# Performance work log

Measured on AMD Instinct MI355X. Metric: run time of the kernel, lower is better.

The kernel has to match this reference:

```python
import jax, jax.numpy as jnp
import numpy as np

DIM = 128
HEADS = 8
HEAD_DIM = DIM // HEADS
PE_DIM = 48
TEMP = 10000.0
WIN = 2
NUM_VALUES = WIN * WIN
SCALE = HEAD_DIM ** -0.5
TWO_PI = 2.0 * np.pi
EPS = 1e-6


def _interleave_sincos(p):
    # p [..., nf] -> interleaved sin(even)/cos(odd), matching torch stack+flatten
    s = jnp.sin(p[..., 0::2])
    c = jnp.cos(p[..., 1::2])
    return jnp.stack((s, c), axis=-1).reshape(p.shape)


def _dim_t(num_pos_feats):
    i = np.arange(num_pos_feats)
    return jnp.asarray(TEMP ** (2.0 * (i // 2) / num_pos_feats), dtype=jnp.float32)


def window_position_bias():
    nf = PE_DIM // 2
    ye = jnp.arange(WIN, dtype=jnp.float32)  # cumsum(ones)-1 along h
    xe = jnp.arange(WIN, dtype=jnp.float32)
    ye = ye / (ye[-1] + EPS) * TWO_PI
    xe = xe / (xe[-1] + EPS) * TWO_PI
    dt = _dim_t(nf)
    pos_y = ye[:, None, None] / dt
    pos_x = xe[None, :, None] / dt
    pos_y = jnp.broadcast_to(pos_y, (WIN, WIN, nf))
    pos_x = jnp.broadcast_to(pos_x, (WIN, WIN, nf))
    pe = jnp.concatenate((_interleave_sincos(pos_y), _interleave_sincos(pos_x)), axis=-1)
    return pe.reshape(NUM_VALUES, PE_DIM)


def points_position_encoding(points):
    # points [n, hw, 2] fractional offsets -> [n, hw, PE_DIM]
    nf = PE_DIM // 2
    ye = points[..., 0] / (WIN + EPS) * TWO_PI
    xe = points[..., 1] / (WIN + EPS) * TWO_PI
    dt = _dim_t(nf)
    pos_y = _interleave_sincos(ye[..., None] / dt)
    pos_x = _interleave_sincos(xe[..., None] / dt)
    return jnp.concatenate((pos_y, pos_x), axis=-1)


def setup_inputs() -> dict:
    key = jax.random.key(0)
    ks = jax.random.split(key, 12)
    n, c, h, w = 2, 48, 192, 192
    y = jax.random.normal(ks[0], (n, c, h, w), jnp.float32)
    x = jax.random.normal(ks[1], (n, c, h, w), jnp.float32)
    conv_w = jax.random.normal(ks[2], (1, 2 * PE_DIM, 3, 3), jnp.float32) * 0.05
    conv_b = jnp.zeros((1,), jnp.float32)
    q_w = jax.random.normal(ks[3], (PE_DIM, DIM), jnp.float32) * (PE_DIM ** -0.5)
    q_b = jnp.zeros((DIM,), jnp.float32)
    k_w = jax.random.normal(ks[4], (PE_DIM, DIM), jnp.float32) * (PE_DIM ** -0.5)
    k_b = jnp.zeros((DIM,), jnp.float32)
    v_w = jax.random.normal(ks[5], (PE_DIM, DIM), jnp.float32) * (PE_DIM ** -0.5)
    v_b = jnp.zeros((DIM,), jnp.float32)
    return {"y": y, "x": x, "conv_w": conv_w, "conv_b": conv_b,
            "q_w": q_w, "q_b": q_b, "k_w": k_w, "k_b": k_b, "v_w": v_w, "v_b": v_b}


def reference(y, x, conv_w, conv_b, q_w, q_b, k_w, k_b, v_w, v_b):
    n, c, h, w = x.shape
    hw = h * w
    # per-pixel horizontal offset from both feature maps
    off = jax.lax.conv_general_dilated(
        jnp.concatenate([y, x], axis=1), conv_w, (1, 1), ((1, 1), (1, 1)),
        dimension_numbers=("NCHW", "OIHW", "NCHW")) + conv_b[None, :, None, None]
    off = jnp.transpose(off, (0, 2, 3, 1)) * (2.0 / w)  # [n,h,w,1]

    gh, gw = jnp.meshgrid(jnp.arange(h, dtype=x.dtype), jnp.arange(w, dtype=x.dtype), indexing="ij")
    # flow.flip(-1) puts the offset on the w coordinate only
    grid_wrp = jnp.stack(
        (jnp.broadcast_to(gh, (n, h, w)),
         gw[None] + off[..., 0]), axis=-1)                      # [n,h,w,2]
    flr = jnp.floor(grid_wrp)
    frac = (grid_wrp - flr).reshape(n, hw, 2)
    flr = flr.reshape(n, hw, 2)

    widx = jnp.array([[0, 0], [0, 1], [1, 0], [1, 1]], dtype=x.dtype)  # window_idx_offset
    g4 = (flr[:, :, None, :] + widx).reshape(n, hw * NUM_VALUES, 2)

    idx0 = jnp.clip(g4[..., 0], 0, h - 1).astype(jnp.int32)
    idx1 = jnp.clip(g4[..., 1], 0, w - 1).astype(jnp.int32)
    lin = idx1 + w * idx0                                      # [n, hw*4]
    wrp = jnp.take_along_axis(y.reshape(n, c, hw), lin[:, None, :], axis=2)  # [n,c,hw*4]
    wrp = jnp.transpose(wrp, (0, 2, 1))                        # [n, hw*4, c]

    # pe_dim // c == 1 tiling; add window position bias per pixel
    pb = window_position_bias()                                # [4, PE_DIM]
    wrp = (wrp.reshape(n, hw, NUM_VALUES, PE_DIM) + pb).reshape(n, hw * NUM_VALUES, PE_DIM)

    x_flat = jnp.transpose(x.reshape(n, c, hw), (0, 2, 1))     # [n, hw, c]
    x_in = x_flat + points_position_encoding(frac)

    nhw = n * hw
    q = (x_in @ q_w + q_b).reshape(nhw, HEADS, HEAD_DIM)
    k = (wrp @ k_w + k_b).reshape(nhw, NUM_VALUES, HEADS, HEAD_DIM)
    v = (wrp @ v_w + v_b).reshape(nhw, NUM_VALUES, HEADS, HEAD_DIM)

    attn = jnp.einsum("phd,pkhd->phk", q * SCALE, k)           # [nhw, heads, 4]
    attn = jax.nn.softmax(attn, axis=-1)
    out = jnp.einsum("phk,pkhd->phd", attn, v).reshape(nhw, DIM)
    return jnp.transpose(out.reshape(n, h, w, DIM), (0, 3, 1, 2))
```

## Files before the change

### kernel.cpp

```cpp
#include <hip/hip_runtime.h>
#include <hip/hip_bf16.h>

#define HW_ 36864
#define W_ 192
#define H_ 192
#define NPIX_ 73728
#define TWO_PI_F 6.283185307179586f

typedef __attribute__((ext_vector_type(8))) short bfrag;
typedef __attribute__((ext_vector_type(4))) float f4;

__device__ __constant__ float DT_G[12] = {
    1.0f, 2.154434690031884f, 4.641588833612779f, 10.0f,
    21.54434690031884f, 46.41588833612779f, 100.0f, 215.4434690031884f,
    464.1588833612779f, 1000.0f, 2154.434690031884f, 4641.588833612779f};

__device__ __forceinline__ unsigned short f2bf(float f) {
    __hip_bfloat16 h = __float2bfloat16(f);
    unsigned short u;
    __builtin_memcpy(&u, &h, 2);
    return u;
}

__device__ __forceinline__ int a_idx(int tile, int m, int k) {
    return tile * 1024 + ((k >> 5) << 9) + (m << 3) + (((k >> 3) & 3) << 7) + (k & 7);
}

__device__ __forceinline__ int rsw(int r) { return ((r & 3) << 2) | (r >> 2); }

__device__ __forceinline__ float red16(float v) {
    int t;
    t = __builtin_amdgcn_update_dpp(0, __float_as_int(v), 0x128, 0xF, 0xF, true);
    v += __int_as_float(t);
    t = __builtin_amdgcn_update_dpp(0, __float_as_int(v), 0x124, 0xF, 0xF, true);
    v += __int_as_float(t);
    t = __builtin_amdgcn_update_dpp(0, __float_as_int(v), 0x122, 0xF, 0xF, true);
    v += __int_as_float(t);
    t = __builtin_amdgcn_update_dpp(0, __float_as_int(v), 0x121, 0xF, 0xF, true);
    v += __int_as_float(t);
    return v;
}

__global__ void prep_wfrag(const float* __restrict__ qw, const float* __restrict__ kw,
                           const float* __restrict__ vw, unsigned short* __restrict__ wsb) {
    int idx = blockIdx.x * 256 + threadIdx.x;
    if (idx >= 24576) return;
    int j = idx & 7;
    int lane = (idx >> 3) & 63;
    int ks = (idx >> 9) & 1;
    int h = (idx >> 10) & 7;
    int mat = idx >> 13;
    const float* w = (mat == 0) ? qw : (mat == 1) ? kw : vw;
    int k = ks * 32 + ((lane >> 4) << 3) + j;
    int n = (h << 4) + (lane & 15);
    float f = (k < 48) ? w[k * 128 + n] : 0.0f;
    wsb[idx] = f2bf(f);
}

struct __align__(16) Smem {
    unsigned short A[10 * 1024];
    float outt[128 * 33];
    float pbl[192];
    float offs[32];
    float part[8][32];
};

__global__ __launch_bounds__(512, 4) void fused_kernel(
    const float* __restrict__ y, const float* __restrict__ x,
    const float* __restrict__ cw, const float* __restrict__ cb,
    const float* __restrict__ qb, const float* __restrict__ kb,
    const float* __restrict__ vb, const unsigned short* __restrict__ wsb,
    float* __restrict__ out) {
    __shared__ Smem sm;
    int tid = threadIdx.x;
    int bid = blockIdx.x;
    int b = (bid & 7) * 288 + (bid >> 3);
    int pix0 = b * 32;
    int n = pix0 / HW_;
    int rem0 = pix0 - n * HW_;
    int row0 = rem0 / W_;
    int col0 = rem0 - row0 * W_;

    float xv8[8];
    if (tid < 256) {
        int p = tid & 31, q = tid >> 5;
        int col = col0 + p;
        float m_lf = (col > 0) ? 1.f : 0.f, m_rt = (col < W_ - 1) ? 1.f : 0.f;
        float m_up = (row0 > 0) ? 1.f : 0.f, m_dn = (row0 < H_ - 1) ? 1.f : 0.f;
        int c_lf = col - (col > 0 ? 1 : 0);
        int c_rt = col + (col < W_ - 1 ? 1 : 0);
        int r_up = row0 - (row0 > 0 ? 1 : 0);
        int r_dn = row0 + (row0 < H_ - 1 ? 1 : 0);
        float k0 = m_up * m_lf, k1 = m_up, k2 = m_up * m_rt;
        float k3 = m_lf, k5 = m_rt;
        float k6 = m_dn * m_lf, k7 = m_dn, k8 = m_dn * m_rt;
        int icbase = (q >> 1) * 24 + (q & 1) * 12;
        float acc = 0.f;
#pragma unroll
        for (int g2 = 0; g2 < 4; ++g2) {
            float buf[27];
#pragma unroll
            for (int cc = 0; cc < 3; ++cc) {
                int ic = icbase + g2 * 3 + cc;
                const float* src = (ic < 48) ? y : x;
                int c = (ic < 48) ? ic : ic - 48;
                const float* b0p = src + (size_t)(n * 48 + c) * HW_;
                const float* pu = b0p + (size_t)r_up * W_;
                const float* pm = b0p + (size_t)row0 * W_;
                const float* pd = b0p + (size_t)r_dn * W_;
                buf[cc * 9 + 0] = pu[c_lf];
                buf[cc * 9 + 1] = pu[col];
                buf[cc * 9 + 2] = pu[c_rt];
                buf[cc * 9 + 3] = pm[c_lf];
                buf[cc * 9 + 4] = pm[col];
                buf[cc * 9 + 5] = pm[c_rt];
                buf[cc * 9 + 6] = pd[c_lf];
                buf[cc * 9 + 7] = pd[col];
                buf[cc * 9 + 8] = pd[c_rt];
            }
#pragma unroll
            for (int cc = 0; cc < 3; ++cc) {
                int ic = icbase + g2 * 3 + cc;
                const float* wp = cw + ic * 9;
                acc += buf[cc * 9 + 0] * (wp[0] * k0);
                acc += buf[cc * 9 + 1] * (wp[1] * k1);
                acc += buf[cc * 9 + 2] * (wp[2] * k2);
                acc += buf[cc * 9 + 3] * (wp[3] * k3);
                acc += buf[cc * 9 + 4] * wp[4];
                acc += buf[cc * 9 + 5] * (wp[5] * k5);
                acc += buf[cc * 9 + 6] * (wp[6] * k6);
                acc += buf[cc * 9 + 7] * (wp[7] * k7);
                acc += buf[cc * 9 + 8] * (wp[8] * k8);
            }
        }
        sm.part[q][p] = acc;
    } else {
        int e = tid - 256, p = e & 31, oct = e >> 5;
        if (oct < 6) {
            const float* xb = x + (size_t)(n * 48 + oct * 8) * HW_ + rem0 + p;
#pragma unroll
            for (int j = 0; j < 8; ++j) xv8[j] = xb[(size_t)j * HW_];
        }
        if (e < 192) {
            int v = e / 48, c = e - (e / 48) * 48;
            int iy = v >> 1, ix = v & 1;
            int cc = (c < 24) ? c : c - 24;
            int sel = (c < 24) ? iy : ix;
            float ee = sel ? (TWO_PI_F / (1.0f + 1e-6f)) : 0.0f;
            float arg = ee / DT_G[cc >> 1];
            sm.pbl[v * 48 + c] = (cc & 1) ? __cosf(arg) : __sinf(arg);
        }
    }
    __syncthreads();
    if (tid < 32) {
        float a = sm.part[0][tid];
#pragma unroll
        for (int s = 1; s < 8; ++s) a += sm.part[s][tid];
        sm.offs[tid] = (a + cb[0]) * (2.0f / (float)W_);
    }
    __syncthreads();

    float yv[16];
    int r_w = tid & 127, oct_w = tid >> 7, t_w = 0, m_w = 0, v_w = 0;
    bool do_wrp = tid < 384;
    if (do_wrp) {
        int p = r_w >> 2;
        v_w = r_w & 3;
        float o = sm.offs[p];
        float gx = (float)(col0 + p) + o;
        float fx = floorf(gx);
        int dy = v_w >> 1, dx = v_w & 1;
        int rr = (int)fminf(fmaxf((float)(row0 + dy), 0.0f), 191.0f);
        int ccx = (int)fminf(fmaxf(fx + (float)dx, 0.0f), 191.0f);
        const float* yb = y + (size_t)(n * 48) * HW_ + (size_t)rr * W_ + ccx;
#pragma unroll
        for (int j = 0; j < 8; ++j) yv[j] = yb[(size_t)(oct_w * 8 + j) * HW_];
#pragma unroll
        for (int j = 0; j < 8; ++j) yv[8 + j] = yb[(size_t)((oct_w + 3) * 8 + j) * HW_];
        t_w = 2 + (r_w >> 4);
        m_w = r_w & 15;
    }
    if (tid >= 256) {
        int e = tid - 256, p = e & 31, oct = e >> 5;
        bfrag w0;
        if (oct < 6) {
            float o = sm.offs[p];
            float gx = (float)(col0 + p) + o;
            float fr = gx - floorf(gx);
            float t1 = fr / (2.0f + 1e-6f);
#pragma unroll
            for (int j = 0; j < 8; ++j) {
                float pe;
                if (oct < 3) {
                    pe = (j & 1) ? 1.0f : 0.0f;
                } else {
                    int cc = oct * 8 + j - 24;
                    float arg = (t1 * TWO_PI_F) / DT_G[cc >> 1];
                    pe = (cc & 1) ? __cosf(arg) : __sinf(arg);
                }
                w0[j] = (short)f2bf(xv8[j] + pe);
            }
        } else {
#pragma unroll
            for (int j = 0; j < 8; ++j) w0[j] = 0;
        }
        *(bfrag*)&sm.A[a_idx(p >> 4, rsw(p & 15), oct * 8)] = w0;
    } else {
        int r = tid & 127, o2 = 6 + (tid >> 7);
        bfrag z;
#pragma unroll
        for (int j = 0; j < 8; ++j) z[j] = 0;
        *(bfrag*)&sm.A[a_idx(2 + (r >> 4), r & 15, o2 * 8)] = z;
    }
    if (do_wrp) {
        bfrag w0, w1;
#pragma unroll
        for (int j = 0; j < 8; ++j)
            w0[j] = (short)f2bf(yv[j] + sm.pbl[v_w * 48 + oct_w * 8 + j]);
#pragma unroll
        for (int j = 0; j < 8; ++j)
            w1[j] = (short)f2bf(yv[8 + j] + sm.pbl[v_w * 48 + (oct_w + 3) * 8 + j]);
        *(bfrag*)&sm.A[a_idx(t_w, m_w, oct_w * 8)] = w0;
        *(bfrag*)&sm.A[a_idx(t_w, m_w, (oct_w + 3) * 8)] = w1;
    }
    __syncthreads();

    int lane = tid & 63, h = tid >> 6;
    int lq = lane & 15, lg = lane >> 4;
    float qbv = qb[(h << 4) + lq];
    float kbv = kb[(h << 4) + lq];
    float vbv = vb[(h << 4) + lq];

    const int hb = (h << 1) * 64 + lane;
    bfrag qB0 = *(const bfrag*)&wsb[(0 * 1024 + hb) * 8];
    bfrag qB1 = *(const bfrag*)&wsb[(0 * 1024 + hb + 64) * 8];
    bfrag kB0 = *(const bfrag*)&wsb[(1 * 1024 + hb) * 8];
    bfrag kB1 = *(const bfrag*)&wsb[(1 * 1024 + hb + 64) * 8];
    bfrag vB0 = *(const bfrag*)&wsb[(2 * 1024 + hb) * 8];
    bfrag vB1 = *(const bfrag*)&wsb[(2 * 1024 + hb + 64) * 8];

    f4 qacc[2];
#pragma unroll
    for (int t = 0; t < 2; ++t) {
        bfrag a0 = *(const bfrag*)&sm.A[t * 1024 + lane * 8];
        bfrag a1 = *(const bfrag*)&sm.A[t * 1024 + 512 + lane * 8];
        f4 a = {qbv, qbv, qbv, qbv};
        a = __builtin_amdgcn_mfma_f32_16x16x32_bf16(a0, qB0, a, 0, 0, 0);
        a = __builtin_amdgcn_mfma_f32_16x16x32_bf16(a1, qB1, a, 0, 0, 0);
        qacc[t] = a;
    }

#pragma unroll
    for (int m = 0; m < 8; ++m) {
        bfrag a0 = *(const bfrag*)&sm.A[(2 + m) * 1024 + lane * 8];
        bfrag a1 = *(const bfrag*)&sm.A[(2 + m) * 1024 + 512 + lane * 8];
        f4 ka = {kbv, kbv, kbv, kbv};
        ka = __builtin_amdgcn_mfma_f32_16x16x32_bf16(a0, kB0, ka, 0, 0, 0);
        ka = __builtin_amdgcn_mfma_f32_16x16x32_bf16(a1, kB1, ka, 0, 0, 0);
        f4 va = {vbv, vbv, vbv, vbv};
        va = __builtin_amdgcn_mfma_f32_16x16x32_bf16(a0, vB0, va, 0, 0, 0);
        va = __builtin_amdgcn_mfma_f32_16x16x32_bf16(a1, vB1, va, 0, 0, 0);

        f4 qa = qacc[m >> 2];
        float qv = ((m & 3) == 0) ? qa.x : ((m & 3) == 1) ? qa.y
                 : ((m & 3) == 2) ? qa.z : qa.w;
        qv *= 0.25f;

        float s0 = qv * ka.x, s1 = qv * ka.y, s2 = qv * ka.z, s3 = qv * ka.w;
        s0 = red16(s0);
        s1 = red16(s1);
        s2 = red16(s2);
        s3 = red16(s3);
        float mx = fmaxf(fmaxf(s0, s1), fmaxf(s2, s3));
        float e0 = __expf(s0 - mx), e1 = __expf(s1 - mx);
        float e2 = __expf(s2 - mx), e3 = __expf(s3 - mx);
        float rden = 1.0f / (e0 + e1 + e2 + e3);
        float o = (e0 * va.x + e1 * va.y + e2 * va.z + e3 * va.w) * rden;
        sm.outt[((h << 4) + lq) * 33 + (m << 2) + lg] = o;
    }
    __syncthreads();

    {
        int ch = tid >> 2, q4 = tid & 3;
        const float* sp = &sm.outt[ch * 33 + q4 * 8];
        float4* dst = (float4*)(out + (size_t)(n * 128 + ch) * HW_ + rem0 + q4 * 8);
        dst[0] = make_float4(sp[0], sp[1], sp[2], sp[3]);
        dst[1] = make_float4(sp[4], sp[5], sp[6], sp[7]);
    }
}

extern "C" void kernel_launch(void* const* d_in, const int* in_sizes, int n_in,
                              void* d_out, int out_size, void* d_ws, size_t ws_size,
                              hipStream_t stream) {
    unsigned short* wsb = (unsigned short*)d_ws;
    hipLaunchKernelGGL(prep_wfrag, dim3(96), dim3(256), 0, stream,
                       (const float*)d_in[4], (const float*)d_in[6],
                       (const float*)d_in[8], wsb);
    hipLaunchKernelGGL(fused_kernel, dim3(NPIX_ / 32), dim3(512), 0, stream,
                       (const float*)d_in[0], (const float*)d_in[1],
                       (const float*)d_in[2], (const float*)d_in[3],
                       (const float*)d_in[5], (const float*)d_in[7],
                       (const float*)d_in[9], wsb,
                       (float*)d_out);
}
```

Before: 135.6 us.

## Fold q scale into weights, add interior conv fast path, prefetch fragments

```diff
diff --git a/kernel.cpp b/kernel.cpp
--- a/kernel.cpp
+++ b/kernel.cpp
@@ -54,6 +54,7 @@
     int k = ks * 32 + ((lane >> 4) << 3) + j;
     int n = (h << 4) + (lane & 15);
     float f = (k < 48) ? w[k * 128 + n] : 0.0f;
+    if (mat == 0) f *= 0.25f;
     wsb[idx] = f2bf(f);
 }
 
@@ -65,7 +66,7 @@
     float part[8][32];
 };
 
-__global__ __launch_bounds__(512, 4) void fused_kernel(
+__global__ __launch_bounds__(512, 8) void fused_kernel(
     const float* __restrict__ y, const float* __restrict__ x,
     const float* __restrict__ cw, const float* __restrict__ cb,
     const float* __restrict__ qb, const float* __restrict__ kb,
@@ -85,15 +86,19 @@
     if (tid < 256) {
         int p = tid & 31, q = tid >> 5;
         int col = col0 + p;
-        float m_lf = (col > 0) ? 1.f : 0.f, m_rt = (col < W_ - 1) ? 1.f : 0.f;
-        float m_up = (row0 > 0) ? 1.f : 0.f, m_dn = (row0 < H_ - 1) ? 1.f : 0.f;
+        bool border = (col0 == 0) || (col0 + 32 == W_) || (row0 == 0) || (row0 == H_ - 1);
         int c_lf = col - (col > 0 ? 1 : 0);
         int c_rt = col + (col < W_ - 1 ? 1 : 0);
         int r_up = row0 - (row0 > 0 ? 1 : 0);
         int r_dn = row0 + (row0 < H_ - 1 ? 1 : 0);
-        float k0 = m_up * m_lf, k1 = m_up, k2 = m_up * m_rt;
-        float k3 = m_lf, k5 = m_rt;
-        float k6 = m_dn * m_lf, k7 = m_dn, k8 = m_dn * m_rt;
+        float k0 = 1.f, k1 = 1.f, k2 = 1.f, k3 = 1.f, k5 = 1.f, k6 = 1.f, k7 = 1.f, k8 = 1.f;
+        if (border) {
+            float m_lf = (col > 0) ? 1.f : 0.f, m_rt = (col < W_ - 1) ? 1.f : 0.f;
+            float m_up = (row0 > 0) ? 1.f : 0.f, m_dn = (row0 < H_ - 1) ? 1.f : 0.f;
+            k0 = m_up * m_lf; k1 = m_up; k2 = m_up * m_rt;
+            k3 = m_lf; k5 = m_rt;
+            k6 = m_dn * m_lf; k7 = m_dn; k8 = m_dn * m_rt;
+        }
         int icbase = (q >> 1) * 24 + (q & 1) * 12;
         float acc = 0.f;
 #pragma unroll
@@ -118,19 +123,34 @@
                 buf[cc * 9 + 7] = pd[col];
                 buf[cc * 9 + 8] = pd[c_rt];
             }
-#pragma unroll
-            for (int cc = 0; cc < 3; ++cc) {
-                int ic = icbase + g2 * 3 + cc;
-                const float* wp = cw + ic * 9;
-                acc += buf[cc * 9 + 0] * (wp[0] * k0);
-                acc += buf[cc * 9 + 1] * (wp[1] * k1);
-                acc += buf[cc * 9 + 2] * (wp[2] * k2);
-                acc += buf[cc * 9 + 3] * (wp[3] * k3);
-                acc += buf[cc * 9 + 4] * wp[4];
-                acc += buf[cc * 9 + 5] * (wp[5] * k5);
-                acc += buf[cc * 9 + 6] * (wp[6] * k6);
-                acc += buf[cc * 9 + 7] * (wp[7] * k7);
-                acc += buf[cc * 9 + 8] * (wp[8] * k8);
+            if (!border) {
+#pragma unroll
+                for (int cc = 0; cc < 3; ++cc) {
+                    const float* wp = cw + (icbase + g2 * 3 + cc) * 9;
+                    acc += buf[cc * 9 + 0] * wp[0];
+                    acc += buf[cc * 9 + 1] * wp[1];
+                    acc += buf[cc * 9 + 2] * wp[2];
+                    acc += buf[cc * 9 + 3] * wp[3];
+                    acc += buf[cc * 9 + 4] * wp[4];
+                    acc += buf[cc * 9 + 5] * wp[5];
+                    acc += buf[cc * 9 + 6] * wp[6];
+                    acc += buf[cc * 9 + 7] * wp[7];
+                    acc += buf[cc * 9 + 8] * wp[8];
+                }
+            } else {
+#pragma unroll
+                for (int cc = 0; cc < 3; ++cc) {
+                    const float* wp = cw + (icbase + g2 * 3 + cc) * 9;
+                    acc += buf[cc * 9 + 0] * (wp[0] * k0);
+                    acc += buf[cc * 9 + 1] * (wp[1] * k1);
+                    acc += buf[cc * 9 + 2] * (wp[2] * k2);
+                    acc += buf[cc * 9 + 3] * (wp[3] * k3);
+                    acc += buf[cc * 9 + 4] * wp[4];
+                    acc += buf[cc * 9 + 5] * (wp[5] * k5);
+                    acc += buf[cc * 9 + 6] * (wp[6] * k6);
+                    acc += buf[cc * 9 + 7] * (wp[7] * k7);
+                    acc += buf[cc * 9 + 8] * (wp[8] * k8);
+                }
             }
         }
         sm.part[q][p] = acc;
@@ -159,6 +179,16 @@
         sm.offs[tid] = (a + cb[0]) * (2.0f / (float)W_);
     }
     __syncthreads();
+
+    int lane = tid & 63, h = tid >> 6;
+    int lq = lane & 15, lg = lane >> 4;
+    const int hb = (h << 1) * 64 + lane;
+    bfrag qB0 = *(const bfrag*)&wsb[(0 * 1024 + hb) * 8];
+    bfrag qB1 = *(const bfrag*)&wsb[(0 * 1024 + hb + 64) * 8];
+    bfrag kB0 = *(const bfrag*)&wsb[(1 * 1024 + hb) * 8];
+    bfrag kB1 = *(const bfrag*)&wsb[(1 * 1024 + hb + 64) * 8];
+    bfrag vB0 = *(const bfrag*)&wsb[(2 * 1024 + hb) * 8];
+    bfrag vB1 = *(const bfrag*)&wsb[(2 * 1024 + hb + 64) * 8];
 
     float yv[16];
     int r_w = tid & 127, oct_w = tid >> 7, t_w = 0, m_w = 0, v_w = 0;
@@ -225,19 +255,9 @@
     }
     __syncthreads();
 
-    int lane = tid & 63, h = tid >> 6;
-    int lq = lane & 15, lg = lane >> 4;
-    float qbv = qb[(h << 4) + lq];
+    float qbv = qb[(h << 4) + lq] * 0.25f;
     float kbv = kb[(h << 4) + lq];
     float vbv = vb[(h << 4) + lq];
-
-    const int hb = (h << 1) * 64 + lane;
-    bfrag qB0 = *(const bfrag*)&wsb[(0 * 1024 + hb) * 8];
-    bfrag qB1 = *(const bfrag*)&wsb[(0 * 1024 + hb + 64) * 8];
-    bfrag kB0 = *(const bfrag*)&wsb[(1 * 1024 + hb) * 8];
-    bfrag kB1 = *(const bfrag*)&wsb[(1 * 1024 + hb + 64) * 8];
-    bfrag vB0 = *(const bfrag*)&wsb[(2 * 1024 + hb) * 8];
-    bfrag vB1 = *(const bfrag*)&wsb[(2 * 1024 + hb + 64) * 8];
 
     f4 qacc[2];
 #pragma unroll
@@ -250,21 +270,25 @@
         qacc[t] = a;
     }
 
+    bfrag c0 = *(const bfrag*)&sm.A[2 * 1024 + lane * 8];
+    bfrag c1 = *(const bfrag*)&sm.A[2 * 1024 + 512 + lane * 8];
 #pragma unroll
     for (int m = 0; m < 8; ++m) {
-        bfrag a0 = *(const bfrag*)&sm.A[(2 + m) * 1024 + lane * 8];
-        bfrag a1 = *(const bfrag*)&sm.A[(2 + m) * 1024 + 512 + lane * 8];
+        bfrag n0, n1;
+        if (m < 7) {
+            n0 = *(const bfrag*)&sm.A[(3 + m) * 1024 + lane * 8];
+            n1 = *(const bfrag*)&sm.A[(3 + m) * 1024 + 512 + lane * 8];
+        }
         f4 ka = {kbv, kbv, kbv, kbv};
-        ka = __builtin_amdgcn_mfma_f32_16x16x32_bf16(a0, kB0, ka, 0, 0, 0);
-        ka = __builtin_amdgcn_mfma_f32_16x16x32_bf16(a1, kB1, ka, 0, 0, 0);
+        ka = __builtin_amdgcn_mfma_f32_16x16x32_bf16(c0, kB0, ka, 0, 0, 0);
+        ka = __builtin_amdgcn_mfma_f32_16x16x32_bf16(c1, kB1, ka, 0, 0, 0);
         f4 va = {vbv, vbv, vbv, vbv};
-        va = __builtin_amdgcn_mfma_f32_16x16x32_bf16(a0, vB0, va, 0, 0, 0);
-        va = __builtin_amdgcn_mfma_f32_16x16x32_bf16(a1, vB1, va, 0, 0, 0);
+        va = __builtin_amdgcn_mfma_f32_16x16x32_bf16(c0, vB0, va, 0, 0, 0);
+        va = __builtin_amdgcn_mfma_f32_16x16x32_bf16(c1, vB1, va, 0, 0, 0);
 
         f4 qa = qacc[m >> 2];
         float qv = ((m & 3) == 0) ? qa.x : ((m & 3) == 1) ? qa.y
                  : ((m & 3) == 2) ? qa.z : qa.w;
-        qv *= 0.25f;
 
         float s0 = qv * ka.x, s1 = qv * ka.y, s2 = qv * ka.z, s3 = qv * ka.w;
         s0 = red16(s0);
@@ -277,6 +301,7 @@
         float rden = 1.0f / (e0 + e1 + e2 + e3);
         float o = (e0 * va.x + e1 * va.y + e2 * va.z + e3 * va.w) * rden;
         sm.outt[((h << 4) + lq) * 33 + (m << 2) + lg] = o;
+        if (m < 7) { c0 = n0; c1 = n1; }
     }
     __syncthreads();
 
```

After: 164.8 us. 21.5% more time.
